# Kernel tuning notes

Hardware: AMD Instinct MI355X
Metric: run time of the kernel (lower is better)

## Reference

```python
import jax, jax.numpy as jnp
import numpy as np

RC = 6.0            # cosine cutoff radius (Angstrom)
N_ANGULAR = 128     # module init arg; output dim = 3*N_ANGULAR
EPS = 1e-12


def cosine_cutoff(d):
    # Behler-style cosine cutoff: 0.5*(cos(pi*d/rc)+1) for d < rc, else 0
    return jnp.where(d < RC, 0.5 * (jnp.cos(jnp.pi * d / RC) + 1.0), 0.0)


def setup_inputs() -> dict:
    key = jax.random.key(0)
    k1, k2, k3, k4 = jax.random.split(key, 4)
    B, N, M = 8, 4096, 96
    L = 20.0  # box length
    positions = jax.random.uniform(k1, (B, N, 3), dtype=jnp.float32) * L
    cell = jnp.tile(jnp.eye(3, dtype=jnp.float32) * L, (B, 1, 1))
    neighbors = jax.random.randint(k2, (B, N, M), 0, N, dtype=jnp.int32)
    offsets = jax.random.randint(k3, (B, N, M, 3), -1, 2).astype(jnp.float32)
    mask = (jax.random.uniform(k4, (B, N, M)) > 0.1).astype(jnp.float32)
    return {"positions": positions, "cell": cell, "offsets": offsets,
            "mask": mask, "neighbors": neighbors}


def reference(positions, cell, offsets, mask, neighbors):
    B, N, M = neighbors.shape
    # gather neighbor positions: pos_j[b,n,m,:] = positions[b, neighbors[b,n,m], :]
    idx = neighbors.reshape(B, N * M)
    pos_j = jnp.take_along_axis(positions, idx[:, :, None], axis=1).reshape(B, N, M, 3)
    # displacement vectors with periodic offsets (offsets in cell coordinates)
    dis_vec = pos_j - positions[:, :, None, :] + jnp.einsum('bnmi,bij->bnmj', offsets, cell)
    distances = jnp.sqrt(jnp.sum(dis_vec * dis_vec, axis=-1) + EPS)  # [B,N,M]
    # cutoff / distance, zeroed where mask == 0
    cut = jnp.where(mask != 0.0, cosine_cutoff(distances) / distances, 0.0)
    # sort neighbors by descending cut value, gather cut-weighted vectors in that order
    order = jnp.argsort(-cut, axis=-1)                       # [B,N,M]
    cut_vec = cut[..., None] * dis_vec                       # [B,N,M,3]
    cut_vec = jnp.take_along_axis(cut_vec, order[..., None], axis=2)
    cut_vec = cut_vec.reshape(B, N, M * 3)
    # scatter into zero-padded descriptor of width 3*n_angular
    f = jnp.zeros((B, N, N_ANGULAR * 3), dtype=positions.dtype)
    f = f.at[:, :, : M * 3].set(cut_vec)
    return f
```

## Files before the change

### kernel.cpp

```cpp
#include <hip/hip_runtime.h>
#include <math.h>

#define M_NB   96
#define OUT_W  384
#define NATOM  4096
#define WPB    16
#define NITER  4

__device__ __forceinline__ void merge3(float4& a4, float2& a2, int base,
                                       float v0, float v1, float v2, int lane)
{
    const int f4lo = 4 * lane;
    const int f2lo = 256 + 2 * lane;
    const float v[3] = {v0, v1, v2};
    #pragma unroll
    for (int t = 0; t < 3; ++t) {
        const int idx = base + t;
        if      (idx == f4lo)     a4.x = v[t];
        else if (idx == f4lo + 1) a4.y = v[t];
        else if (idx == f4lo + 2) a4.z = v[t];
        else if (idx == f4lo + 3) a4.w = v[t];
        else if (idx == f2lo)     a2.x = v[t];
        else if (idx == f2lo + 1) a2.y = v[t];
    }
}

__global__ __launch_bounds__(64 * WPB, 8) void deepmd_angular_kernel(
    const float* __restrict__ positions,
    const float* __restrict__ cell,
    const float* __restrict__ offsets,
    const float* __restrict__ mask,
    const int*   __restrict__ neighbors,
    float*       __restrict__ out,
    int N)
{
    __shared__ float4 pos4_s[NATOM];

    const int tid  = threadIdx.x;
    const int wv   = tid >> 6;
    const int lane = tid & 63;
    const bool low = lane < 32;

    const int p0 = blockIdx.x * (WPB * NITER);
    const int b  = p0 / N;

    {
        const float* pb_ = positions + (size_t)b * N * 3;
        for (int a = tid; a < NATOM; a += 64 * WPB) {
            const float3 v = *(const float3*)(pb_ + 3 * a);
            pos4_s[a] = make_float4(v.x, v.y, v.z, 0.f);
        }
    }
    __syncthreads();

    const float* cb = cell + (size_t)b * 9;
    const float c00 = cb[0], c01 = cb[1], c02 = cb[2];
    const float c10 = cb[3], c11 = cb[4], c12 = cb[5];
    const float c20 = cb[6], c21 = cb[7], c22 = cb[8];

    #pragma unroll
    for (int it = 0; it < NITER; ++it) {
        const int q  = p0 + wv * NITER + it;
        const int nn = q - b * N;

        const long eA = (long)q * M_NB + lane;
        const int    jA = neighbors[eA];
        const float mkA = mask[eA];
        const float3 oA = *(const float3*)(offsets + eA * 3);

        int jB = 0; float mkB = 0.f; float3 oB = make_float3(0.f, 0.f, 0.f);
        if (low) {
            const long eB = eA + 64;
            jB  = neighbors[eB];
            mkB = mask[eB];
            oB  = *(const float3*)(offsets + eB * 3);
        }

        const float4 pi  = pos4_s[nn];
        const float4 pjA = pos4_s[jA];

        const float dxA = pjA.x - pi.x + oA.x * c00 + oA.y * c10 + oA.z * c20;
        const float dyA = pjA.y - pi.y + oA.x * c01 + oA.y * c11 + oA.z * c21;
        const float dzA = pjA.z - pi.z + oA.x * c02 + oA.y * c12 + oA.z * c22;
        const float dA  = sqrtf(dxA * dxA + dyA * dyA + dzA * dzA + 1e-12f);
        float cutA = 0.f;
        if (mkA != 0.f && dA < 6.f)
            cutA = 0.5f * (__cosf(dA * 0.52359877559829887f) + 1.f) / dA;

        float dxB = 0.f, dyB = 0.f, dzB = 0.f, cutB = 0.f;
        if (low) {
            const float4 pjB = pos4_s[jB];
            dxB = pjB.x - pi.x + oB.x * c00 + oB.y * c10 + oB.z * c20;
            dyB = pjB.y - pi.y + oB.x * c01 + oB.y * c11 + oB.z * c21;
            dzB = pjB.z - pi.z + oB.x * c02 + oB.y * c12 + oB.z * c22;
            const float dB = sqrtf(dxB * dxB + dyB * dyB + dzB * dzB + 1e-12f);
            if (mkB != 0.f && dB < 6.f)
                cutB = 0.5f * (__cosf(dB * 0.52359877559829887f) + 1.f) / dB;
        }

        const float w0A = cutA * dxA, w1A = cutA * dyA, w2A = cutA * dzA;
        const float w0B = cutB * dxB, w1B = cutB * dyB, w2B = cutB * dzB;

        float4 a4 = make_float4(0.f, 0.f, 0.f, 0.f);
        float2 a2 = make_float2(0.f, 0.f);

        unsigned long long t = __ballot(cutA != 0.f);
        while (t) {
            const int s = (int)__builtin_ctzll(t); t &= t - 1;
            const float c = __shfl(cutA, s);
            const unsigned long long gtA = __ballot(cutA > c);
            const unsigned long long gtB = __ballot(cutB > c);
            const unsigned long long eqA = __ballot(cutA == c);
            const int rank = __popcll(gtA) + __popcll(gtB)
                           + __popcll(eqA & ((1ull << s) - 1ull));
            merge3(a4, a2, 3 * rank,
                   __shfl(w0A, s), __shfl(w1A, s), __shfl(w2A, s), lane);
        }
        t = __ballot(cutB != 0.f);
        while (t) {
            const int s = (int)__builtin_ctzll(t); t &= t - 1;
            const float c = __shfl(cutB, s);
            const unsigned long long gtA = __ballot(cutA > c);
            const unsigned long long gtB = __ballot(cutB > c);
            const unsigned long long eqA = __ballot(cutA == c);
            const unsigned long long eqB = __ballot(cutB == c);
            const int rank = __popcll(gtA) + __popcll(gtB) + __popcll(eqA)
                           + __popcll(eqB & ((1ull << s) - 1ull));
            merge3(a4, a2, 3 * rank,
                   __shfl(w0B, s), __shfl(w1B, s), __shfl(w2B, s), lane);
        }

        float* rowp = out + (size_t)q * OUT_W;
        ((float4*)rowp)[lane] = a4;
        ((float2*)(rowp + 256))[lane] = a2;
    }
}

extern "C" void kernel_launch(void* const* d_in, const int* in_sizes, int n_in,
                              void* d_out, int out_size, void* d_ws, size_t ws_size,
                              hipStream_t stream) {
    const float* positions = (const float*)d_in[0];
    const float* cell      = (const float*)d_in[1];
    const float* offsets   = (const float*)d_in[2];
    const float* mask      = (const float*)d_in[3];
    const int*   neighbors = (const int*)d_in[4];
    float*       out       = (float*)d_out;

    const int BN = in_sizes[0] / 3;
    const int B  = in_sizes[1] / 9;
    const int N  = BN / B;

    dim3 block(64 * WPB, 1, 1);
    dim3 grid(BN / (WPB * NITER), 1, 1);
    deepmd_angular_kernel<<<grid, block, 0, stream>>>(
        positions, cell, offsets, mask, neighbors, out, N);
}
```

Measured before the change: 118.4 us.

## Pack two atoms' 192 neighbors into three full wavefront slots

The old code had each wavefront handle one atom's 96 neighbors as 64 plus 32 lanes, leaving half the lanes idle on the second pass. The new code gives each wavefront two atoms at once, spreading their 192 neighbors over three fully used 64-lane registers. The middle register is split by lane-half masks so each atom is ranked and merged on its own. This keeps lanes busy during loads, distance math and cutoff evaluation, at the cost of more ballot masking and more registers.

```diff
diff --git a/kernel.cpp b/kernel.cpp
--- a/kernel.cpp
+++ b/kernel.cpp
@@ -5,7 +5,8 @@
 #define OUT_W  384
 #define NATOM  4096
 #define WPB    16
-#define NITER  4
+#define LOWM   0x00000000FFFFFFFFull
+#define HIGHM  0xFFFFFFFF00000000ull
 
 __device__ __forceinline__ void merge3(float4& a4, float2& a2, int base,
                                        float v0, float v1, float v2, int lane)
@@ -39,9 +40,8 @@
     const int tid  = threadIdx.x;
     const int wv   = tid >> 6;
     const int lane = tid & 63;
-    const bool low = lane < 32;
 
-    const int p0 = blockIdx.x * (WPB * NITER);
+    const int p0 = blockIdx.x * (WPB * 4);
     const int b  = p0 / N;
 
     {
@@ -59,80 +59,105 @@
     const float c20 = cb[6], c21 = cb[7], c22 = cb[8];
 
     #pragma unroll
-    for (int it = 0; it < NITER; ++it) {
-        const int q  = p0 + wv * NITER + it;
-        const int nn = q - b * N;
+    for (int it = 0; it < 2; ++it) {
+        const int q0   = p0 + wv * 4 + it * 2;
+        const long base = (long)q0 * M_NB;
+        const long e0 = base + lane, e1 = e0 + 64, e2 = e0 + 128;
 
-        const long eA = (long)q * M_NB + lane;
-        const int    jA = neighbors[eA];
-        const float mkA = mask[eA];
-        const float3 oA = *(const float3*)(offsets + eA * 3);
+        const int   j0 = neighbors[e0], j1 = neighbors[e1], j2 = neighbors[e2];
+        const float m0 = mask[e0],      m1 = mask[e1],      m2 = mask[e2];
+        const float3 o0 = *(const float3*)(offsets + e0 * 3);
+        const float3 o1 = *(const float3*)(offsets + e1 * 3);
+        const float3 o2 = *(const float3*)(offsets + e2 * 3);
 
-        int jB = 0; float mkB = 0.f; float3 oB = make_float3(0.f, 0.f, 0.f);
-        if (low) {
-            const long eB = eA + 64;
-            jB  = neighbors[eB];
-            mkB = mask[eB];
-            oB  = *(const float3*)(offsets + eB * 3);
-        }
+        const int nn0 = q0 - b * N;
+        const float4 pi0 = pos4_s[nn0];
+        const float4 pi1 = pos4_s[nn0 + 1];
+        const float4 pj0 = pos4_s[j0];
+        const float4 pj1 = pos4_s[j1];
+        const float4 pj2 = pos4_s[j2];
+        const float4 pa  = (lane < 32) ? pi0 : pi1;
 
-        const float4 pi  = pos4_s[nn];
-        const float4 pjA = pos4_s[jA];
+        float w0x = pj0.x - pi0.x + o0.x * c00 + o0.y * c10 + o0.z * c20;
+        float w0y = pj0.y - pi0.y + o0.x * c01 + o0.y * c11 + o0.z * c21;
+        float w0z = pj0.z - pi0.z + o0.x * c02 + o0.y * c12 + o0.z * c22;
+        float d   = sqrtf(w0x * w0x + w0y * w0y + w0z * w0z + 1e-12f);
+        float c0v = 0.f;
+        if (m0 != 0.f && d < 6.f)
+            c0v = 0.5f * (__cosf(d * 0.52359877559829887f) + 1.f) / d;
+        w0x *= c0v; w0y *= c0v; w0z *= c0v;
 
-        const float dxA = pjA.x - pi.x + oA.x * c00 + oA.y * c10 + oA.z * c20;
-        const float dyA = pjA.y - pi.y + oA.x * c01 + oA.y * c11 + oA.z * c21;
-        const float dzA = pjA.z - pi.z + oA.x * c02 + oA.y * c12 + oA.z * c22;
-        const float dA  = sqrtf(dxA * dxA + dyA * dyA + dzA * dzA + 1e-12f);
-        float cutA = 0.f;
-        if (mkA != 0.f && dA < 6.f)
-            cutA = 0.5f * (__cosf(dA * 0.52359877559829887f) + 1.f) / dA;
+        float w1x = pj1.x - pa.x + o1.x * c00 + o1.y * c10 + o1.z * c20;
+        float w1y = pj1.y - pa.y + o1.x * c01 + o1.y * c11 + o1.z * c21;
+        float w1z = pj1.z - pa.z + o1.x * c02 + o1.y * c12 + o1.z * c22;
+        d = sqrtf(w1x * w1x + w1y * w1y + w1z * w1z + 1e-12f);
+        float c1v = 0.f;
+        if (m1 != 0.f && d < 6.f)
+            c1v = 0.5f * (__cosf(d * 0.52359877559829887f) + 1.f) / d;
+        w1x *= c1v; w1y *= c1v; w1z *= c1v;
 
-        float dxB = 0.f, dyB = 0.f, dzB = 0.f, cutB = 0.f;
-        if (low) {
-            const float4 pjB = pos4_s[jB];
-            dxB = pjB.x - pi.x + oB.x * c00 + oB.y * c10 + oB.z * c20;
-            dyB = pjB.y - pi.y + oB.x * c01 + oB.y * c11 + oB.z * c21;
-            dzB = pjB.z - pi.z + oB.x * c02 + oB.y * c12 + oB.z * c22;
-            const float dB = sqrtf(dxB * dxB + dyB * dyB + dzB * dzB + 1e-12f);
-            if (mkB != 0.f && dB < 6.f)
-                cutB = 0.5f * (__cosf(dB * 0.52359877559829887f) + 1.f) / dB;
-        }
-
-        const float w0A = cutA * dxA, w1A = cutA * dyA, w2A = cutA * dzA;
-        const float w0B = cutB * dxB, w1B = cutB * dyB, w2B = cutB * dzB;
+        float w2x = pj2.x - pi1.x + o2.x * c00 + o2.y * c10 + o2.z * c20;
+        float w2y = pj2.y - pi1.y + o2.x * c01 + o2.y * c11 + o2.z * c21;
+        float w2z = pj2.z - pi1.z + o2.x * c02 + o2.y * c12 + o2.z * c22;
+        d = sqrtf(w2x * w2x + w2y * w2y + w2z * w2z + 1e-12f);
+        float c2v = 0.f;
+        if (m2 != 0.f && d < 6.f)
+            c2v = 0.5f * (__cosf(d * 0.52359877559829887f) + 1.f) / d;
+        w2x *= c2v; w2y *= c2v; w2z *= c2v;
 
         float4 a4 = make_float4(0.f, 0.f, 0.f, 0.f);
         float2 a2 = make_float2(0.f, 0.f);
-
-        unsigned long long t = __ballot(cutA != 0.f);
+        unsigned long long t = __ballot(c0v != 0.f);
         while (t) {
             const int s = (int)__builtin_ctzll(t); t &= t - 1;
-            const float c = __shfl(cutA, s);
-            const unsigned long long gtA = __ballot(cutA > c);
-            const unsigned long long gtB = __ballot(cutB > c);
-            const unsigned long long eqA = __ballot(cutA == c);
-            const int rank = __popcll(gtA) + __popcll(gtB)
-                           + __popcll(eqA & ((1ull << s) - 1ull));
+            const float c = __shfl(c0v, s);
+            const int rank = __popcll(__ballot(c0v > c))
+                           + __popcll(__ballot(c1v > c) & LOWM)
+                           + __popcll(__ballot(c0v == c) & ((1ull << s) - 1ull));
             merge3(a4, a2, 3 * rank,
-                   __shfl(w0A, s), __shfl(w1A, s), __shfl(w2A, s), lane);
+                   __shfl(w0x, s), __shfl(w0y, s), __shfl(w0z, s), lane);
         }
-        t = __ballot(cutB != 0.f);
+        t = __ballot(c1v != 0.f) & LOWM;
         while (t) {
             const int s = (int)__builtin_ctzll(t); t &= t - 1;
-            const float c = __shfl(cutB, s);
-            const unsigned long long gtA = __ballot(cutA > c);
-            const unsigned long long gtB = __ballot(cutB > c);
-            const unsigned long long eqA = __ballot(cutA == c);
-            const unsigned long long eqB = __ballot(cutB == c);
-            const int rank = __popcll(gtA) + __popcll(gtB) + __popcll(eqA)
-                           + __popcll(eqB & ((1ull << s) - 1ull));
+            const float c = __shfl(c1v, s);
+            const int rank = __popcll(__ballot(c0v > c))
+                           + __popcll(__ballot(c1v > c) & LOWM)
+                           + __popcll(__ballot(c0v == c))
+                           + __popcll(__ballot(c1v == c) & LOWM & ((1ull << s) - 1ull));
             merge3(a4, a2, 3 * rank,
-                   __shfl(w0B, s), __shfl(w1B, s), __shfl(w2B, s), lane);
+                   __shfl(w1x, s), __shfl(w1y, s), __shfl(w1z, s), lane);
         }
+        float* row0 = out + (size_t)q0 * OUT_W;
+        ((float4*)row0)[lane] = a4;
+        ((float2*)(row0 + 256))[lane] = a2;
 
-        float* rowp = out + (size_t)q * OUT_W;
-        ((float4*)rowp)[lane] = a4;
-        ((float2*)(rowp + 256))[lane] = a2;
+        float4 b4 = make_float4(0.f, 0.f, 0.f, 0.f);
+        float2 b2 = make_float2(0.f, 0.f);
+        t = __ballot(c1v != 0.f) & HIGHM;
+        while (t) {
+            const int s = (int)__builtin_ctzll(t); t &= t - 1;
+            const float c = __shfl(c1v, s);
+            const int rank = __popcll(__ballot(c1v > c) & HIGHM)
+                           + __popcll(__ballot(c2v > c))
+                           + __popcll(__ballot(c1v == c) & HIGHM & ((1ull << s) - 1ull));
+            merge3(b4, b2, 3 * rank,
+                   __shfl(w1x, s), __shfl(w1y, s), __shfl(w1z, s), lane);
+        }
+        t = __ballot(c2v != 0.f);
+        while (t) {
+            const int s = (int)__builtin_ctzll(t); t &= t - 1;
+            const float c = __shfl(c2v, s);
+            const int rank = __popcll(__ballot(c1v > c) & HIGHM)
+                           + __popcll(__ballot(c2v > c))
+                           + __popcll(__ballot(c1v == c) & HIGHM)
+                           + __popcll(__ballot(c2v == c) & ((1ull << s) - 1ull));
+            merge3(b4, b2, 3 * rank,
+                   __shfl(w2x, s), __shfl(w2y, s), __shfl(w2z, s), lane);
+        }
+        float* row1 = out + (size_t)(q0 + 1) * OUT_W;
+        ((float4*)row1)[lane] = b4;
+        ((float2*)(row1 + 256))[lane] = b2;
     }
 }
 
@@ -151,7 +176,7 @@
     const int N  = BN / B;
 
     dim3 block(64 * WPB, 1, 1);
-    dim3 grid(BN / (WPB * NITER), 1, 1);
+    dim3 grid(BN / (WPB * 4), 1, 1);
     deepmd_angular_kernel<<<grid, block, 0, stream>>>(
         positions, cell, offsets, mask, neighbors, out, N);
 }
```

Measured after the change: 115.3 us. 1.03x faster.
